# Optimization experiments

Measured on AMD Instinct MI355X. Metric: run time of the kernel, lower is better.

The kernel has to match this reference:

```python
import jax, jax.numpy as jnp
import numpy as np

CHANNELS = 256
CODEBOOK_SIZE = 8192
UPDATE_SPEED = 0.01
N_TOKENS = 32768


def setup_inputs() -> dict:
    key = jax.random.key(0)
    k1, k2 = jax.random.split(key)
    embeddings = jax.random.normal(k1, (N_TOKENS, CHANNELS), dtype=jnp.float32)
    code_usage = jnp.ones((CODEBOOK_SIZE,), dtype=jnp.float32)
    code_embedding_sum = jax.random.normal(k2, (CODEBOOK_SIZE, CHANNELS), dtype=jnp.float32)
    return {"embeddings": embeddings, "code_usage": code_usage,
            "code_embedding_sum": code_embedding_sum}


def reference(embeddings, code_usage, code_embedding_sum):
    # codebook from EMA statistics: [K, C]
    codebook = code_embedding_sum / jnp.clip(code_usage, 1e-5, None)[:, None]

    # encode: nearest code by Euclidean distance. argmin over codes is
    # invariant under sqrt, so use squared distances (avoids sqrt of [K, N]).
    cb_sq = jnp.sum(codebook * codebook, axis=-1)            # [K]
    x_sq = jnp.sum(embeddings * embeddings, axis=-1)         # [N]
    # d2[k, n] = ||cb_k - x_n||^2
    d2 = cb_sq[:, None] - 2.0 * jnp.einsum('kc,nc->kn', codebook, embeddings) + x_sq[None, :]
    codes = jnp.argmin(d2, axis=0).astype(jnp.int32)         # [N]

    # decode: gather codebook rows
    quantized = jnp.take(codebook, codes, axis=0)            # [N, C]

    # straight-through estimator
    embeddings_q = embeddings + jax.lax.stop_gradient(quantized - embeddings)

    # commitment loss: mse(stop_grad(embeddings_q), embeddings)
    diff = jax.lax.stop_gradient(embeddings_q) - embeddings
    commitment_loss = jnp.mean(diff * diff)

    # EMA updates (training mode, under no_grad in the original)
    n = embeddings.shape[0]
    counts = jax.ops.segment_sum(jnp.ones((n,), dtype=code_usage.dtype),
                                 codes, num_segments=CODEBOOK_SIZE)
    emb_sum = jax.ops.segment_sum(embeddings, codes, num_segments=CODEBOOK_SIZE)
    s = jnp.float32(UPDATE_SPEED)
    new_code_usage = jax.lax.stop_gradient(code_usage * (1.0 - s) + counts * s)
    new_code_embedding_sum = jax.lax.stop_gradient(
        code_embedding_sum * (1.0 - s) + emb_sum * s)

    return codes, embeddings_q, commitment_loss, new_code_usage, new_code_embedding_sum
```

## Files before the change

kernel.cpp:

```cpp
#include <hip/hip_runtime.h>

#define CH 256
#define KC 8192
#define NT 32768

#define TM 128
#define TN 128
#define BK 32
#define NSTG ((KC / TN) * (CH / BK))

typedef _Float16 half4_t __attribute__((ext_vector_type(4)));
typedef _Float16 half8_t __attribute__((ext_vector_type(8)));
typedef float floatx4 __attribute__((ext_vector_type(4)));

typedef __attribute__((address_space(1))) const unsigned int guint_t;
typedef __attribute__((address_space(3))) unsigned int luint_t;

__global__ void k_prep(const float* __restrict__ usage,
                       const float* __restrict__ ces,
                       const float* __restrict__ emb,
                       _Float16* __restrict__ cbh,
                       _Float16* __restrict__ cbl,
                       float* __restrict__ cbsq,
                       _Float16* __restrict__ eh,
                       _Float16* __restrict__ el,
                       int* __restrict__ hist) {
    int b = blockIdx.x, t = threadIdx.x;
    if (b < KC) {
        float uc = fmaxf(usage[b], 1e-5f);
        float v  = ces[b * CH + t];
        float cb = v / uc;
        _Float16 h = (_Float16)cb;
        cbh[b * CH + t] = h;
        cbl[b * CH + t] = (_Float16)(cb - (float)h);

        float p = cb * cb;
        #pragma unroll
        for (int off = 32; off; off >>= 1) p += __shfl_down(p, off);
        __shared__ float ps[4];
        int lane = t & 63, w = t >> 6;
        if (lane == 0) ps[w] = p;
        __syncthreads();
        if (t == 0) cbsq[b] = ps[0] + ps[1] + ps[2] + ps[3];
        if (t == 1) hist[b] = 0;
    } else {
        int i = (b - KC) * 256 + t;
        float4 v = ((const float4*)emb)[i];
        float va[4] = {v.x, v.y, v.z, v.w};
        half4_t h, l;
        #pragma unroll
        for (int q = 0; q < 4; ++q) {
            _Float16 hh = (_Float16)va[q];
            h[q] = hh;
            l[q] = (_Float16)(va[q] - (float)hh);
        }
        ((half4_t*)eh)[i] = h;
        ((half4_t*)el)[i] = l;
    }
}

__launch_bounds__(256, 1)
__global__ void k_argmin(const _Float16* __restrict__ eh,
                         const _Float16* __restrict__ el,
                         const _Float16* __restrict__ cbh,
                         const _Float16* __restrict__ cbl,
                         const float* __restrict__ cbsq,
                         unsigned long long* __restrict__ packed) {
    __shared__ __align__(16) unsigned char smraw[163840];
    _Float16* smA = (_Float16*)smraw;

    const int t    = threadIdx.x;
    const int lane = t & 63;
    const int wave = t >> 6;
    const int wx   = wave;
    const int lr   = lane & 15;
    const int koq  = lane >> 4;
    const int lrow4 = lane >> 2;
    const int ch4   = lane & 3;

    const int n0 = blockIdx.x * TM;

    char*      smBw  = (char*)smraw + 131072 + wave * 8192;
    _Float16*  smBwh = (_Float16*)smBw;

    float minv[32];
    int   mini[32];
    #pragma unroll
    for (int e = 0; e < 32; ++e) { minv[e] = 3.402823466e38f; mini[e] = 0; }

    floatx4 acc[8][2];
    #pragma unroll
    for (int mf = 0; mf < 8; ++mf) {
        acc[mf][0] = (floatx4){0.f, 0.f, 0.f, 0.f};
        acc[mf][1] = (floatx4){0.f, 0.f, 0.f, 0.f};
    }

    auto dmaB = [&](int buf, int sg) {
        const int c0 = (sg & 7) * BK;
        const int jb = (sg >> 3) * TN + wx * 32;
        const _Float16* gh = cbh + (size_t)(jb + lrow4) * CH + c0 + ch4 * 8;
        const _Float16* gl = cbl + (size_t)(jb + lrow4) * CH + c0 + ch4 * 8;
        char* d = smBw + buf * 4096;
        __builtin_amdgcn_global_load_lds((guint_t*)gh,
                                         (luint_t*)(d), 16, 0, 0);
        __builtin_amdgcn_global_load_lds((guint_t*)(gh + 16 * CH),
                                         (luint_t*)(d + 1024), 16, 0, 0);
        __builtin_amdgcn_global_load_lds((guint_t*)gl,
                                         (luint_t*)(d + 2048), 16, 0, 0);
        __builtin_amdgcn_global_load_lds((guint_t*)(gl + 16 * CH),
                                         (luint_t*)(d + 3072), 16, 0, 0);
    };

    {
        const int hl  = wave >> 1;
        const int ccb = (wave & 1) * 4;
        const _Float16* a_hl = hl ? el : eh;
        #pragma unroll
        for (int d = 0; d < 4; ++d) {
            const int cc = ccb + d;
            #pragma unroll
            for (int p = 0; p < 8; ++p) {
                const _Float16* g = a_hl + (size_t)(n0 + p * 16 + lrow4) * CH
                                  + cc * 32 + ch4 * 8;
                __builtin_amdgcn_global_load_lds(
                    (guint_t*)g,
                    (luint_t*)(smraw + hl * 65536 + cc * 8192 + p * 1024),
                    16, 0, 0);
            }
        }
    }
    dmaB(0, 0);
    dmaB(1, 1);
    asm volatile("s_waitcnt vmcnt(0)" ::: "memory");
    __syncthreads();

    half8_t fah[2][8], fal[2][8], fbh[2][2], fbl[2][2];
    float csq0 = 0.f, csq1 = 0.f;

    {
        const int ab = lr * 32 + koq * 8;
        #pragma unroll
        for (int mf = 0; mf < 8; ++mf) {
            fah[0][mf] = *(const half8_t*)&smA[ab + mf * 512];
            fal[0][mf] = *(const half8_t*)&smA[32768 + ab + mf * 512];
        }
        const int bb = lr * 32 + koq * 8;
        fbh[0][0] = *(const half8_t*)&smBwh[bb];
        fbh[0][1] = *(const half8_t*)&smBwh[bb + 512];
        fbl[0][0] = *(const half8_t*)&smBwh[bb + 1024];
        fbl[0][1] = *(const half8_t*)&smBwh[bb + 1536];
    }

#define SUBITER(S_, FC, FN, BUFD, BUFR, DO_CSQ, DO_FOLD)                     \
  {                                                                          \
    const int S = (S_);                                                      \
    asm volatile("s_waitcnt vmcnt(0) lgkmcnt(0)" ::: "memory");              \
    if (S + 2 < NSTG) dmaB((BUFD), S + 2);                                   \
    if (DO_CSQ && (S & 7) == 0) {                                            \
      const int jb0 = (S >> 3) * TN + wx * 32 + lr;                          \
      csq0 = cbsq[jb0];                                                      \
      csq1 = cbsq[jb0 + 16];                                                 \
    }                                                                        \
    if (S + 1 < NSTG) {                                                      \
      const int ccn = (S + 1) & 7;                                           \
      const int ab  = ccn * 4096 + lr * 32 + koq * 8;                        \
      _Pragma("unroll")                                                      \
      for (int mf = 0; mf < 8; ++mf) {                                       \
        fah[FN][mf] = *(const half8_t*)&smA[ab + mf * 512];                  \
        fal[FN][mf] = *(const half8_t*)&smA[32768 + ab + mf * 512];          \
      }                                                                      \
      const int bb = (BUFR) * 2048 + lr * 32 + koq * 8;                      \
      fbh[FN][0] = *(const half8_t*)&smBwh[bb];                              \
      fbh[FN][1] = *(const half8_t*)&smBwh[bb + 512];                        \
      fbl[FN][0] = *(const half8_t*)&smBwh[bb + 1024];                       \
      fbl[FN][1] = *(const half8_t*)&smBwh[bb + 1536];                       \
    }                                                                        \
    _Pragma("unroll")                                                        \
    for (int mf = 0; mf < 8; ++mf) {                                         \
      acc[mf][0] = __builtin_amdgcn_mfma_f32_16x16x32_f16(                   \
          fah[FC][mf], fbh[FC][0], acc[mf][0], 0, 0, 0);                     \
      acc[mf][1] = __builtin_amdgcn_mfma_f32_16x16x32_f16(                   \
          fah[FC][mf], fbh[FC][1], acc[mf][1], 0, 0, 0);                     \
    }                                                                        \
    _Pragma("unroll")                                                        \
    for (int mf = 0; mf < 8; ++mf) {                                         \
      acc[mf][0] = __builtin_amdgcn_mfma_f32_16x16x32_f16(                   \
          fah[FC][mf], fbl[FC][0], acc[mf][0], 0, 0, 0);                     \
      acc[mf][1] = __builtin_amdgcn_mfma_f32_16x16x32_f16(                   \
          fah[FC][mf], fbl[FC][1], acc[mf][1], 0, 0, 0);                     \
    }                                                                        \
    _Pragma("unroll")                                                        \
    for (int mf = 0; mf < 8; ++mf) {                                         \
      acc[mf][0] = __builtin_amdgcn_mfma_f32_16x16x32_f16(                   \
          fal[FC][mf], fbh[FC][0], acc[mf][0], 0, 0, 0);                     \
      acc[mf][1] = __builtin_amdgcn_mfma_f32_16x16x32_f16(                   \
          fal[FC][mf], fbh[FC][1], acc[mf][1], 0, 0, 0);                     \
    }                                                                        \
    if (DO_FOLD && (S & 7) == 7) {                                           \
      const int jb7 = (S >> 3) * TN + wx * 32 + lr;                          \
      _Pragma("unroll")                                                      \
      for (int mf = 0; mf < 8; ++mf) {                                       \
        _Pragma("unroll")                                                    \
        for (int r = 0; r < 4; ++r) {                                        \
          const int e = mf * 4 + r;                                          \
          float s0 = csq0 - 2.0f * acc[mf][0][r];                            \
          float s1 = csq1 - 2.0f * acc[mf][1][r];                            \
          float sv = s0; int si = jb7;                                       \
          if (s1 < sv) { sv = s1; si = jb7 + 16; }                           \
          if (sv < minv[e]) { minv[e] = sv; mini[e] = si; }                  \
          acc[mf][0][r] = 0.f;                                               \
          acc[mf][1][r] = 0.f;                                               \
        }                                                                    \
      }                                                                      \
    }                                                                        \
  }

    #pragma unroll 1
    for (int sp = 0; sp < NSTG; sp += 2) {
        SUBITER(sp,     0, 1, 0, 1, 1, 0);
        SUBITER(sp + 1, 1, 0, 1, 0, 0, 1);
    }
#undef SUBITER

    __syncthreads();
    float* cand_v = (float*)(smraw + 131072);
    int*   cand_i = (int*)(smraw + 131072 + 2048);

    #pragma unroll
    for (int e = 0; e < 32; ++e) {
        float v = minv[e];
        int   x = mini[e];
        #pragma unroll
        for (int m = 1; m <= 8; m <<= 1) {
            float ov = __shfl_xor(v, m, 64);
            int   ox = __shfl_xor(x, m, 64);
            if (ov < v || (ov == v && ox < x)) { v = ov; x = ox; }
        }
        if (lr == 0) {
            int row = (e >> 2) * 16 + koq * 4 + (e & 3);
            cand_v[wx * TM + row] = v;
            cand_i[wx * TM + row] = x;
        }
    }
    __syncthreads();

    if (t < TM) {
        float v0 = cand_v[t];          int i0 = cand_i[t];
        #pragma unroll
        for (int q = 1; q < 4; ++q) {
            float v1 = cand_v[q * TM + t]; int i1 = cand_i[q * TM + t];
            if (v1 < v0 || (v1 == v0 && i1 < i0)) { v0 = v1; i0 = i1; }
        }
        unsigned sb = __float_as_uint(v0);
        sb = (sb & 0x80000000u) ? ~sb : (sb | 0x80000000u);
        packed[n0 + t] = ((unsigned long long)sb << 32) | (unsigned)i0;
    }
}

__global__ void k_gather(const float* __restrict__ emb,
                         const float* __restrict__ ces,
                         const float* __restrict__ usage,
                         const unsigned long long* __restrict__ packed,
                         float* __restrict__ out_eq,
                         float* __restrict__ codes_f,
                         int* __restrict__ hist,
                         float* __restrict__ partials) {
    int t = threadIdx.x;
    int wave = t >> 6, lane = t & 63;
    int n = blockIdx.x * 4 + wave;
    int k = (int)(packed[n] & 0xFFFFFFFFull);
    float uc = fmaxf(usage[k], 1e-5f);
    int c = lane * 4;

    float4 e = *(const float4*)&emb[(size_t)n * CH + c];
    float4 v = *(const float4*)&ces[(size_t)k * CH + c];
    float ea[4] = {e.x, e.y, e.z, e.w};
    float va[4] = {v.x, v.y, v.z, v.w};
    float eqa[4];
    float p = 0.0f;
    #pragma unroll
    for (int q = 0; q < 4; ++q) {
        float cb = va[q] / uc;
        float eq = ea[q] + (cb - ea[q]);
        eqa[q] = eq;
        float d = eq - ea[q];
        p += d * d;
    }
    *(float4*)&out_eq[(size_t)n * CH + c] =
        (float4){eqa[0], eqa[1], eqa[2], eqa[3]};

    #pragma unroll
    for (int off = 32; off; off >>= 1) p += __shfl_down(p, off);
    __shared__ float ps[4];
    if (lane == 0) {
        ps[wave] = p;
        codes_f[n] = (float)k;
        atomicAdd(&hist[k], 1);
    }
    __syncthreads();
    if (t == 0) partials[blockIdx.x] = ps[0] + ps[1] + ps[2] + ps[3];
}

__global__ void k_scan(const int* __restrict__ hist,
                       int* __restrict__ offs,
                       int* __restrict__ cursor) {
    __shared__ int bs[256];
    int t = threadIdx.x;
    int base = t * 32;
    int loc[32];
    int s = 0;
    #pragma unroll
    for (int i = 0; i < 32; ++i) { loc[i] = s; s += hist[base + i]; }
    int mysum = s;
    bs[t] = s;
    __syncthreads();
    for (int off = 1; off < 256; off <<= 1) {
        int v = (t >= off) ? bs[t - off] : 0;
        __syncthreads();
        bs[t] += v;
        __syncthreads();
    }
    int excl = bs[t] - mysum;
    #pragma unroll
    for (int i = 0; i < 32; ++i) {
        int o = excl + loc[i];
        offs[base + i]   = o;
        cursor[base + i] = o;
    }
}

__global__ void k_scatter(const unsigned long long* __restrict__ packed,
                          int* __restrict__ cursor,
                          int* __restrict__ bucket) {
    int n = blockIdx.x * 256 + threadIdx.x;
    int k = (int)(packed[n] & 0xFFFFFFFFull);
    int pos = atomicAdd(&cursor[k], 1);
    bucket[pos] = n;
}

__global__ void k_ema(const float* __restrict__ emb,
                      const float* __restrict__ ces,
                      const float* __restrict__ usage,
                      const int* __restrict__ hist,
                      const int* __restrict__ offs,
                      const int* __restrict__ bucket,
                      float* __restrict__ out_ces,
                      float* __restrict__ out_usage) {
    const float s = 0.01f;
    const float oms = 1.0f - s;
    int k = blockIdx.x, t = threadIdx.x;
    int start = offs[k], cnt = hist[k];
    float sum = 0.0f;
    #pragma unroll 2
    for (int i = 0; i < cnt; ++i) {
        int n = bucket[start + i];
        sum += emb[(size_t)n * CH + t];
    }
    out_ces[(size_t)k * CH + t] = oms * ces[(size_t)k * CH + t] + s * sum;
    if (t == 0) out_usage[k] = oms * usage[k] + s * (float)cnt;
}

__global__ void k_final(const float* __restrict__ partials,
                        float* __restrict__ out_loss) {
    int t = threadIdx.x;
    float p = 0.0f;
    for (int i = t; i < NT / 4; i += 256) p += partials[i];
    #pragma unroll
    for (int off = 32; off; off >>= 1) p += __shfl_down(p, off);
    __shared__ float ps[4];
    if ((t & 63) == 0) ps[t >> 6] = p;
    __syncthreads();
    if (t == 0)
        out_loss[0] = (ps[0] + ps[1] + ps[2] + ps[3]) * (1.0f / 8388608.0f);
}

extern "C" void kernel_launch(void* const* d_in, const int* in_sizes, int n_in,
                              void* d_out, int out_size, void* d_ws, size_t ws_size,
                              hipStream_t stream) {
    const float* emb   = (const float*)d_in[0];
    const float* usage = (const float*)d_in[1];
    const float* ces   = (const float*)d_in[2];

    float* out      = (float*)d_out;
    float* o_codes  = out;
    float* o_eq     = out + NT;
    float* o_loss   = o_eq + (size_t)NT * CH;
    float* o_usage  = o_loss + 1;
    float* o_ces    = o_usage + KC;

    unsigned long long* packed = (unsigned long long*)d_ws;
    float* cbsq     = (float*)(packed + NT);
    float* partials = cbsq + KC;
    int* hist   = (int*)(partials + NT / 4);
    int* offs   = hist + KC;
    int* cursor = offs + KC;
    int* bucket = cursor + KC;
    _Float16* eh  = (_Float16*)(bucket + NT);
    _Float16* el  = eh + (size_t)NT * CH;
    _Float16* cbh = el + (size_t)NT * CH;
    _Float16* cbl = cbh + (size_t)KC * CH;

    k_prep<<<KC + NT * CH / 1024, 256, 0, stream>>>(
        usage, ces, emb, cbh, cbl, cbsq, eh, el, hist);
    k_argmin<<<NT / TM, 256, 0, stream>>>(eh, el, cbh, cbl, cbsq, packed);
    k_gather<<<NT / 4, 256, 0, stream>>>(emb, ces, usage, packed, o_eq,
                                         o_codes, hist, partials);
    k_scan<<<1, 256, 0, stream>>>(hist, offs, cursor);
    k_scatter<<<NT / 256, 256, 0, stream>>>(packed, cursor, bucket);
    k_ema<<<KC, 256, 0, stream>>>(emb, ces, usage, hist, offs, bucket,
                                  o_ces, o_usage);
    k_final<<<1, 256, 0, stream>>>(partials, o_loss);
}
```

Baseline: 645.8 us.

## Use 8 waves per block and load codebook fragments directly from global memory

```diff
diff --git a/kernel.cpp b/kernel.cpp
--- a/kernel.cpp
+++ b/kernel.cpp
@@ -15,6 +15,10 @@
 
 typedef __attribute__((address_space(1))) const unsigned int guint_t;
 typedef __attribute__((address_space(3))) unsigned int luint_t;
+
+__device__ __forceinline__ int swz(int row, int chunk) {
+    return row * BK + ((chunk ^ ((row >> 1) & 3)) << 3);
+}
 
 __global__ void k_prep(const float* __restrict__ usage,
                        const float* __restrict__ ces,
@@ -59,147 +63,123 @@
     }
 }
 
-__launch_bounds__(256, 1)
+__launch_bounds__(512, 1)
 __global__ void k_argmin(const _Float16* __restrict__ eh,
                          const _Float16* __restrict__ el,
                          const _Float16* __restrict__ cbh,
                          const _Float16* __restrict__ cbl,
                          const float* __restrict__ cbsq,
                          unsigned long long* __restrict__ packed) {
-    __shared__ __align__(16) unsigned char smraw[163840];
+    __shared__ __align__(16) unsigned char smraw[135168];
     _Float16* smA = (_Float16*)smraw;
 
     const int t    = threadIdx.x;
     const int lane = t & 63;
     const int wave = t >> 6;
-    const int wx   = wave;
+    const int wx   = wave & 3;
+    const int wy   = wave >> 2;
     const int lr   = lane & 15;
     const int koq  = lane >> 4;
-    const int lrow4 = lane >> 2;
-    const int ch4   = lane & 3;
 
     const int n0 = blockIdx.x * TM;
 
-    char*      smBw  = (char*)smraw + 131072 + wave * 8192;
-    _Float16*  smBwh = (_Float16*)smBw;
-
-    float minv[32];
-    int   mini[32];
-    #pragma unroll
-    for (int e = 0; e < 32; ++e) { minv[e] = 3.402823466e38f; mini[e] = 0; }
-
-    floatx4 acc[8][2];
-    #pragma unroll
-    for (int mf = 0; mf < 8; ++mf) {
+    const int qsw  = (lane & 3) ^ ((lane >> 3) & 3);
+    const int lrow = lane >> 2;
+
+    float minv[16];
+    int   mini[16];
+    #pragma unroll
+    for (int e = 0; e < 16; ++e) { minv[e] = 3.402823466e38f; mini[e] = 0; }
+
+    floatx4 acc[4][2];
+    #pragma unroll
+    for (int mf = 0; mf < 4; ++mf) {
         acc[mf][0] = (floatx4){0.f, 0.f, 0.f, 0.f};
         acc[mf][1] = (floatx4){0.f, 0.f, 0.f, 0.f};
     }
 
-    auto dmaB = [&](int buf, int sg) {
-        const int c0 = (sg & 7) * BK;
-        const int jb = (sg >> 3) * TN + wx * 32;
-        const _Float16* gh = cbh + (size_t)(jb + lrow4) * CH + c0 + ch4 * 8;
-        const _Float16* gl = cbl + (size_t)(jb + lrow4) * CH + c0 + ch4 * 8;
-        char* d = smBw + buf * 4096;
-        __builtin_amdgcn_global_load_lds((guint_t*)gh,
-                                         (luint_t*)(d), 16, 0, 0);
-        __builtin_amdgcn_global_load_lds((guint_t*)(gh + 16 * CH),
-                                         (luint_t*)(d + 1024), 16, 0, 0);
-        __builtin_amdgcn_global_load_lds((guint_t*)gl,
-                                         (luint_t*)(d + 2048), 16, 0, 0);
-        __builtin_amdgcn_global_load_lds((guint_t*)(gl + 16 * CH),
-                                         (luint_t*)(d + 3072), 16, 0, 0);
-    };
-
     {
-        const int hl  = wave >> 1;
-        const int ccb = (wave & 1) * 4;
+        const int hl  = wave >> 2;
+        const int ccb = (wave & 3) * 2;
         const _Float16* a_hl = hl ? el : eh;
         #pragma unroll
-        for (int d = 0; d < 4; ++d) {
+        for (int d = 0; d < 2; ++d) {
             const int cc = ccb + d;
+            const _Float16* g0 = a_hl + (size_t)(n0 + lrow) * CH + cc * BK
+                               + qsw * 8;
             #pragma unroll
-            for (int p = 0; p < 8; ++p) {
-                const _Float16* g = a_hl + (size_t)(n0 + p * 16 + lrow4) * CH
-                                  + cc * 32 + ch4 * 8;
+            for (int i = 0; i < 8; ++i) {
                 __builtin_amdgcn_global_load_lds(
-                    (guint_t*)g,
-                    (luint_t*)(smraw + hl * 65536 + cc * 8192 + p * 1024),
+                    (guint_t*)(g0 + (size_t)(i * 16) * CH),
+                    (luint_t*)&smA[hl * 32768 + cc * 4096 + i * 512],
                     16, 0, 0);
             }
         }
     }
-    dmaB(0, 0);
-    dmaB(1, 1);
     asm volatile("s_waitcnt vmcnt(0)" ::: "memory");
     __syncthreads();
 
-    half8_t fah[2][8], fal[2][8], fbh[2][2], fbl[2][2];
+    auto loadB = [&](half8_t* bh, half8_t* bl, int sg) {
+        const int c0 = (sg & 7) * BK;
+        const int jb = (sg >> 3) * TN + wx * 32 + lr;
+        const _Float16* gh = cbh + (size_t)jb * CH + c0 + koq * 8;
+        const _Float16* gl = cbl + (size_t)jb * CH + c0 + koq * 8;
+        bh[0] = *(const half8_t*)gh;
+        bh[1] = *(const half8_t*)(gh + 16 * CH);
+        bl[0] = *(const half8_t*)gl;
+        bl[1] = *(const half8_t*)(gl + 16 * CH);
+    };
+    auto loadA = [&](half8_t* ah, half8_t* al, int sg) {
+        const int cc = sg & 7;
+        #pragma unroll
+        for (int mf = 0; mf < 4; ++mf) {
+            int off = cc * 4096 + swz(wy * 64 + mf * 16 + lr, koq);
+            ah[mf] = *(const half8_t*)&smA[off];
+            al[mf] = *(const half8_t*)&smA[32768 + off];
+        }
+    };
+
+    half8_t fah[2][4], fal[2][4], fbh[2][2], fbl[2][2];
     float csq0 = 0.f, csq1 = 0.f;
 
-    {
-        const int ab = lr * 32 + koq * 8;
-        #pragma unroll
-        for (int mf = 0; mf < 8; ++mf) {
-            fah[0][mf] = *(const half8_t*)&smA[ab + mf * 512];
-            fal[0][mf] = *(const half8_t*)&smA[32768 + ab + mf * 512];
-        }
-        const int bb = lr * 32 + koq * 8;
-        fbh[0][0] = *(const half8_t*)&smBwh[bb];
-        fbh[0][1] = *(const half8_t*)&smBwh[bb + 512];
-        fbl[0][0] = *(const half8_t*)&smBwh[bb + 1024];
-        fbl[0][1] = *(const half8_t*)&smBwh[bb + 1536];
-    }
-
-#define SUBITER(S_, FC, FN, BUFD, BUFR, DO_CSQ, DO_FOLD)                     \
+    loadB(fbh[0], fbl[0], 0);
+    loadA(fah[0], fal[0], 0);
+
+#define SUBITER(S_, FC, FN)                                                  \
   {                                                                          \
     const int S = (S_);                                                      \
-    asm volatile("s_waitcnt vmcnt(0) lgkmcnt(0)" ::: "memory");              \
-    if (S + 2 < NSTG) dmaB((BUFD), S + 2);                                   \
-    if (DO_CSQ && (S & 7) == 0) {                                            \
+    if (S + 1 < NSTG) loadB(fbh[FN], fbl[FN], S + 1);                        \
+    if ((S & 7) == 0) {                                                      \
       const int jb0 = (S >> 3) * TN + wx * 32 + lr;                          \
       csq0 = cbsq[jb0];                                                      \
       csq1 = cbsq[jb0 + 16];                                                 \
     }                                                                        \
-    if (S + 1 < NSTG) {                                                      \
-      const int ccn = (S + 1) & 7;                                           \
-      const int ab  = ccn * 4096 + lr * 32 + koq * 8;                        \
-      _Pragma("unroll")                                                      \
-      for (int mf = 0; mf < 8; ++mf) {                                       \
-        fah[FN][mf] = *(const half8_t*)&smA[ab + mf * 512];                  \
-        fal[FN][mf] = *(const half8_t*)&smA[32768 + ab + mf * 512];          \
-      }                                                                      \
-      const int bb = (BUFR) * 2048 + lr * 32 + koq * 8;                      \
-      fbh[FN][0] = *(const half8_t*)&smBwh[bb];                              \
-      fbh[FN][1] = *(const half8_t*)&smBwh[bb + 512];                        \
-      fbl[FN][0] = *(const half8_t*)&smBwh[bb + 1024];                       \
-      fbl[FN][1] = *(const half8_t*)&smBwh[bb + 1536];                       \
-    }                                                                        \
+    if (S + 1 < NSTG) loadA(fah[FN], fal[FN], S + 1);                        \
     _Pragma("unroll")                                                        \
-    for (int mf = 0; mf < 8; ++mf) {                                         \
+    for (int mf = 0; mf < 4; ++mf) {                                         \
       acc[mf][0] = __builtin_amdgcn_mfma_f32_16x16x32_f16(                   \
           fah[FC][mf], fbh[FC][0], acc[mf][0], 0, 0, 0);                     \
       acc[mf][1] = __builtin_amdgcn_mfma_f32_16x16x32_f16(                   \
           fah[FC][mf], fbh[FC][1], acc[mf][1], 0, 0, 0);                     \
     }                                                                        \
     _Pragma("unroll")                                                        \
-    for (int mf = 0; mf < 8; ++mf) {                                         \
+    for (int mf = 0; mf < 4; ++mf) {                                         \
       acc[mf][0] = __builtin_amdgcn_mfma_f32_16x16x32_f16(                   \
           fah[FC][mf], fbl[FC][0], acc[mf][0], 0, 0, 0);                     \
       acc[mf][1] = __builtin_amdgcn_mfma_f32_16x16x32_f16(                   \
           fah[FC][mf], fbl[FC][1], acc[mf][1], 0, 0, 0);                     \
     }                                                                        \
     _Pragma("unroll")                                                        \
-    for (int mf = 0; mf < 8; ++mf) {                                         \
+    for (int mf = 0; mf < 4; ++mf) {                                         \
       acc[mf][0] = __builtin_amdgcn_mfma_f32_16x16x32_f16(                   \
           fal[FC][mf], fbh[FC][0], acc[mf][0], 0, 0, 0);                     \
       acc[mf][1] = __builtin_amdgcn_mfma_f32_16x16x32_f16(                   \
           fal[FC][mf], fbh[FC][1], acc[mf][1], 0, 0, 0);                     \
     }                                                                        \
-    if (DO_FOLD && (S & 7) == 7) {                                           \
+    if ((S & 7) == 7) {                                                      \
       const int jb7 = (S >> 3) * TN + wx * 32 + lr;                          \
       _Pragma("unroll")                                                      \
-      for (int mf = 0; mf < 8; ++mf) {                                       \
+      for (int mf = 0; mf < 4; ++mf) {                                       \
         _Pragma("unroll")                                                    \
         for (int r = 0; r < 4; ++r) {                                        \
           const int e = mf * 4 + r;                                          \
@@ -217,17 +197,16 @@
 
     #pragma unroll 1
     for (int sp = 0; sp < NSTG; sp += 2) {
-        SUBITER(sp,     0, 1, 0, 1, 1, 0);
-        SUBITER(sp + 1, 1, 0, 1, 0, 0, 1);
+        SUBITER(sp,     0, 1);
+        SUBITER(sp + 1, 1, 0);
     }
 #undef SUBITER
 
-    __syncthreads();
     float* cand_v = (float*)(smraw + 131072);
     int*   cand_i = (int*)(smraw + 131072 + 2048);
 
     #pragma unroll
-    for (int e = 0; e < 32; ++e) {
+    for (int e = 0; e < 16; ++e) {
         float v = minv[e];
         int   x = mini[e];
         #pragma unroll
@@ -237,7 +216,7 @@
             if (ov < v || (ov == v && ox < x)) { v = ov; x = ox; }
         }
         if (lr == 0) {
-            int row = (e >> 2) * 16 + koq * 4 + (e & 3);
+            int row = wy * 64 + (e >> 2) * 16 + (lane >> 4) * 4 + (e & 3);
             cand_v[wx * TM + row] = v;
             cand_i[wx * TM + row] = x;
         }
@@ -402,7 +381,7 @@
 
     k_prep<<<KC + NT * CH / 1024, 256, 0, stream>>>(
         usage, ces, emb, cbh, cbl, cbsq, eh, el, hist);
-    k_argmin<<<NT / TM, 256, 0, stream>>>(eh, el, cbh, cbl, cbsq, packed);
+    k_argmin<<<NT / TM, 512, 0, stream>>>(eh, el, cbh, cbl, cbsq, packed);
     k_gather<<<NT / 4, 256, 0, stream>>>(emb, ces, usage, packed, o_eq,
                                          o_codes, hist, partials);
     k_scan<<<1, 256, 0, stream>>>(hist, offs, cursor);
```

Result: slower. 691.9 us (+7.1%).
